# Kernel tuning notes

Measured on AMD Instinct MI355X. Metric: run time of the kernel, lower is better.

Reference implementation:

```python
import jax, jax.numpy as jnp
import numpy as np

K, D, E = 2048, 128, 64

def setup_inputs() -> dict:
    key = jax.random.key(0)
    k1, k2, k3 = jax.random.split(key, 3)
    z = jax.random.normal(k1, (K, D), dtype=jnp.float32)
    # Kaiming-like scaling so logits stay in a sane range
    W1 = jax.random.normal(k2, (2 * D, E), dtype=jnp.float32) / jnp.sqrt(2.0 * D)
    b1 = jnp.zeros((E,), dtype=jnp.float32)
    W2 = jax.random.normal(k3, (E, 1), dtype=jnp.float32) / jnp.sqrt(1.0 * E)
    b2 = jnp.zeros((1,), dtype=jnp.float32)
    return {"z": z, "W1": W1, "b1": b1, "W2": W2, "b2": b2}


def reference(z, W1, b1, W2, b2):
    # edge_mlp(cat([z_i, z_j])) == z_i @ W1[:d] + z_j @ W1[d:] + b1  (avoids (k,k,2d) concat)
    d = z.shape[1]
    hi = z @ W1[:d]          # (k, e)  -- contribution of z_i (row/query)
    hj = z @ W1[d:]          # (k, e)  -- contribution of z_j (col/key)
    h = jax.nn.silu(hi[:, None, :] + hj[None, :, :] + b1)   # (k, k, e)
    logits = jnp.einsum('ije,eo->ij', h, W2) + b2[0]         # (k, k)
    return jax.nn.softmax(logits, axis=-1)
```

## Files before the change

### kernel.cpp

```cpp
#include <hip/hip_runtime.h>
#include <cstdint>
#include <cstddef>

#define KTOT 2048
#define DDIM 128
#define EDIM 64
#define RPB  4
#define JR   512
#define KPB  4

#define LOG2E 1.44269504088896f

typedef float v2f __attribute__((ext_vector_type(2)));

__global__ void proj_kernel(const float* __restrict__ z,
                            const float* __restrict__ W1,
                            const float* __restrict__ b1,
                            const float* __restrict__ w2,
                            float* __restrict__ hiw, float* __restrict__ Ei,
                            float* __restrict__ hjw, float* __restrict__ Ej) {
  __shared__ float zrow[KPB][DDIM];
  const int t  = threadIdx.x;
  const int k0 = blockIdx.x * KPB;
#pragma unroll
  for (int r = 0; r < KPB; ++r) zrow[r][t] = z[(size_t)(k0 + r) * DDIM + t];
  __syncthreads();

  const int  e    = t & 63;
  const bool isHj = (t >= 64);
  const float* Wcol = W1 + (isHj ? DDIM * EDIM : 0) + e;

  float acc[KPB];
  const float binit = isHj ? 0.0f : b1[e];
#pragma unroll
  for (int r = 0; r < KPB; ++r) acc[r] = binit;

#pragma unroll 4
  for (int d = 0; d < DDIM; ++d) {
    const float w = Wcol[(size_t)d * EDIM];
#pragma unroll
    for (int r = 0; r < KPB; ++r) acc[r] = fmaf(zrow[r][d], w, acc[r]);
  }

  const float wv = w2[e];
  float* dw = isHj ? hjw : hiw;
  float* dE = isHj ? Ej  : Ei;
#pragma unroll
  for (int r = 0; r < KPB; ++r) {
    const float tv = acc[r] * LOG2E;
    dw[(size_t)(k0 + r) * EDIM + e] = tv * wv;
    dE[(size_t)(k0 + r) * EDIM + e] = __builtin_amdgcn_exp2f(-tv);
  }
}

__device__ __forceinline__ void quad_nd(const float4 hw, const float4 he,
                                        const float4 jw, const float4 je,
                                        float& Nq, float& Dq) {
  const v2f u01 = (v2f){hw.x, hw.y} + (v2f){jw.x, jw.y};
  const v2f u23 = (v2f){hw.z, hw.w} + (v2f){jw.z, jw.w};
  const v2f d01 = (v2f){he.x, he.y} * (v2f){je.x, je.y} + 1.0f;
  const v2f d23 = (v2f){he.z, he.w} * (v2f){je.z, je.w} + 1.0f;
  const float n01 = fmaf(u01.x, d01.y, u01.y * d01.x);
  const float n23 = fmaf(u23.x, d23.y, u23.y * d23.x);
  const float p01 = d01.x * d01.y;
  const float p23 = d23.x * d23.y;
  Nq = fmaf(n01, p23, n23 * p01);
  Dq = p01 * p23;
}

__device__ __forceinline__ float dpp_red8(float a) {
  int t;
  t = __builtin_amdgcn_update_dpp(0, __float_as_int(a), 0xB1, 0xF, 0xF, true);
  a += __int_as_float(t);
  t = __builtin_amdgcn_update_dpp(0, __float_as_int(a), 0x4E, 0xF, 0xF, true);
  a += __int_as_float(t);
  t = __builtin_amdgcn_update_dpp(0, __float_as_int(a), 0x141, 0xF, 0xF, true);
  a += __int_as_float(t);
  return a;
}

__global__ __launch_bounds__(256, 4) void edge_kernel(
    const float* __restrict__ hiw_, const float* __restrict__ Ei_,
    const float* __restrict__ hjw_, const float* __restrict__ Ej_,
    float* __restrict__ out, float* __restrict__ partials) {
  __shared__ float logits[RPB][JR];

  const int tid  = threadIdx.x;
  const int lane = tid & 63;
  const int wave = tid >> 6;
  const int sub  = lane & 7;
  const int jg   = lane >> 3;
  const int ig   = blockIdx.x >> 2;
  const int jq   = blockIdx.x & 3;
  const int i0   = ig * RPB;

  float4 hwA[RPB], hwB[RPB], heA[RPB], heB[RPB];
#pragma unroll
  for (int r = 0; r < RPB; ++r) {
    const size_t o = (size_t)(i0 + r) * EDIM + sub * 8;
    hwA[r] = *reinterpret_cast<const float4*>(hiw_ + o);
    hwB[r] = *reinterpret_cast<const float4*>(hiw_ + o + 4);
    heA[r] = *reinterpret_cast<const float4*>(Ei_ + o);
    heB[r] = *reinterpret_cast<const float4*>(Ei_ + o + 4);
  }

  const int jloc = wave * 8 + jg;
  const float* pjw = hjw_ + (size_t)(jq * JR + jloc) * EDIM + sub * 8;
  const float* pje = Ej_  + (size_t)(jq * JR + jloc) * EDIM + sub * 8;

  float4 jwA = *reinterpret_cast<const float4*>(pjw);
  float4 jwB = *reinterpret_cast<const float4*>(pjw + 4);
  float4 jeA = *reinterpret_cast<const float4*>(pje);
  float4 jeB = *reinterpret_cast<const float4*>(pje + 4);

  for (int it = 0; it < JR / 32; ++it) {
    const float4 cwA = jwA, cwB = jwB, ceA = jeA, ceB = jeB;
    if (it + 1 < JR / 32) {
      const size_t off = (size_t)(it + 1) * 32 * EDIM;
      jwA = *reinterpret_cast<const float4*>(pjw + off);
      jwB = *reinterpret_cast<const float4*>(pjw + off + 4);
      jeA = *reinterpret_cast<const float4*>(pje + off);
      jeB = *reinterpret_cast<const float4*>(pje + off + 4);
    }
    const int j = jloc + it * 32;
#pragma unroll
    for (int r = 0; r < RPB; ++r) {
      float N0, D0, N1, D1;
      quad_nd(hwA[r], heA[r], cwA, ceA, N0, D0);
      quad_nd(hwB[r], heB[r], cwB, ceB, N1, D1);
      const float rD = __builtin_amdgcn_rcpf(D0 * D1);
      float a = fmaf(N0, D1, N1 * D0) * rD;
      a = dpp_red8(a);
      if (sub == 0) logits[r][j] = a;
    }
  }
  __syncthreads();

  float* lrow = logits[wave];
  float ssum = 0.0f;
#pragma unroll
  for (int t = 0; t < 8; ++t) {
    const int k = t * 64 + lane;
    const float ev = __builtin_amdgcn_exp2f(lrow[k]);
    lrow[k] = ev;
    ssum += ev;
  }
#pragma unroll
  for (int off = 32; off; off >>= 1) ssum += __shfl_xor(ssum, off);
  if (lane == 0) partials[(size_t)(i0 + wave) * 4 + jq] = ssum;

  float* orow = out + (size_t)(i0 + wave) * KTOT + jq * JR;
#pragma unroll
  for (int t = 0; t < 2; ++t) {
    const int k4 = t * 64 + lane;
    *reinterpret_cast<float4*>(&orow[k4 * 4]) =
        *reinterpret_cast<const float4*>(&lrow[k4 * 4]);
  }
}

__global__ __launch_bounds__(256) void norm_kernel(
    const float* __restrict__ partials, float* __restrict__ out) {
  const int idx = blockIdx.x * 256 + threadIdx.x;
#pragma unroll
  for (int t = 0; t < 4; ++t) {
    const int i4  = idx + t * (1024 * 256);
    const int row = i4 >> 9;
    const float s = (partials[row * 4 + 0] + partials[row * 4 + 1]) +
                    (partials[row * 4 + 2] + partials[row * 4 + 3]);
    const float rinv = __builtin_amdgcn_rcpf(s);
    float4 v = reinterpret_cast<const float4*>(out)[i4];
    v.x *= rinv; v.y *= rinv; v.z *= rinv; v.w *= rinv;
    reinterpret_cast<float4*>(out)[i4] = v;
  }
}

extern "C" void kernel_launch(void* const* d_in, const int* in_sizes, int n_in,
                              void* d_out, int out_size, void* d_ws, size_t ws_size,
                              hipStream_t stream) {
  const float* z  = (const float*)d_in[0];
  const float* W1 = (const float*)d_in[1];
  const float* b1 = (const float*)d_in[2];
  const float* W2 = (const float*)d_in[3];
  float* out = (float*)d_out;

  float* hiw = (float*)d_ws;
  float* Ei  = hiw + (size_t)KTOT * EDIM;
  float* hjw = Ei  + (size_t)KTOT * EDIM;
  float* Ej  = hjw + (size_t)KTOT * EDIM;
  float* partials = Ej + (size_t)KTOT * EDIM;

  hipLaunchKernelGGL(proj_kernel, dim3(KTOT / KPB), dim3(DDIM), 0, stream,
                     z, W1, b1, W2, hiw, Ei, hjw, Ej);
  hipLaunchKernelGGL(edge_kernel, dim3((KTOT / RPB) * 4), dim3(256), 0, stream,
                     hiw, Ei, hjw, Ej, out, partials);
  hipLaunchKernelGGL(norm_kernel, dim3(1024), dim3(256), 0, stream,
                     partials, out);
}
```

Baseline: 62.32 us.

## Fuse softmax normalization into edge kernel with full-row blocks

Each block now covers 2 complete rows across all 2048 columns instead of 4 rows over a quarter of the columns. The block computes the exponentials inline, accumulates per-row sums in registers and shared memory, then rescales its own rows in place, so the separate norm kernel and partials buffer go away. This removes one launch and a full extra read/write pass over the 16 MB output. In exchange, the hj/Ej data is reloaded per 2 rows instead of per 4, which doubles L2 traffic. Output writes also become scattered scalar stores instead of coalesced float4 stores through LDS.

```diff
diff --git a/kernel.cpp b/kernel.cpp
--- a/kernel.cpp
+++ b/kernel.cpp
@@ -5,8 +5,7 @@
 #define KTOT 2048
 #define DDIM 128
 #define EDIM 64
-#define RPB  4
-#define JR   512
+#define RPB  2
 #define KPB  4
 
 #define LOG2E 1.44269504088896f
@@ -82,17 +81,15 @@
 __global__ __launch_bounds__(256, 4) void edge_kernel(
     const float* __restrict__ hiw_, const float* __restrict__ Ei_,
     const float* __restrict__ hjw_, const float* __restrict__ Ej_,
-    float* __restrict__ out, float* __restrict__ partials) {
-  __shared__ float logits[RPB][JR];
+    float* __restrict__ out) {
+  __shared__ float ps[4][RPB];
 
   const int tid  = threadIdx.x;
   const int lane = tid & 63;
   const int wave = tid >> 6;
   const int sub  = lane & 7;
   const int jg   = lane >> 3;
-  const int ig   = blockIdx.x >> 2;
-  const int jq   = blockIdx.x & 3;
-  const int i0   = ig * RPB;
+  const int i0   = blockIdx.x * RPB;
 
   float4 hwA[RPB], hwB[RPB], heA[RPB], heB[RPB];
 #pragma unroll
@@ -105,17 +102,20 @@
   }
 
   const int jloc = wave * 8 + jg;
-  const float* pjw = hjw_ + (size_t)(jq * JR + jloc) * EDIM + sub * 8;
-  const float* pje = Ej_  + (size_t)(jq * JR + jloc) * EDIM + sub * 8;
+  const float* pjw = hjw_ + (size_t)jloc * EDIM + sub * 8;
+  const float* pje = Ej_  + (size_t)jloc * EDIM + sub * 8;
 
   float4 jwA = *reinterpret_cast<const float4*>(pjw);
   float4 jwB = *reinterpret_cast<const float4*>(pjw + 4);
   float4 jeA = *reinterpret_cast<const float4*>(pje);
   float4 jeB = *reinterpret_cast<const float4*>(pje + 4);
 
-  for (int it = 0; it < JR / 32; ++it) {
+  float ssum[RPB] = {0.0f, 0.0f};
+  float* orow0 = out + (size_t)i0 * KTOT;
+
+  for (int it = 0; it < KTOT / 32; ++it) {
     const float4 cwA = jwA, cwB = jwB, ceA = jeA, ceB = jeB;
-    if (it + 1 < JR / 32) {
+    if (it + 1 < KTOT / 32) {
       const size_t off = (size_t)(it + 1) * 32 * EDIM;
       jwA = *reinterpret_cast<const float4*>(pjw + off);
       jwB = *reinterpret_cast<const float4*>(pjw + off + 4);
@@ -131,46 +131,32 @@
       const float rD = __builtin_amdgcn_rcpf(D0 * D1);
       float a = fmaf(N0, D1, N1 * D0) * rD;
       a = dpp_red8(a);
-      if (sub == 0) logits[r][j] = a;
+      const float ev = __builtin_amdgcn_exp2f(a);
+      ssum[r] += ev;
+      if (sub == 0) orow0[(size_t)r * KTOT + j] = ev;
     }
+  }
+
+#pragma unroll
+  for (int r = 0; r < RPB; ++r)
+#pragma unroll
+    for (int off = 32; off; off >>= 1) ssum[r] += __shfl_xor(ssum[r], off);
+  if (lane == 0) {
+#pragma unroll
+    for (int r = 0; r < RPB; ++r) ps[wave][r] = ssum[r];
   }
   __syncthreads();
 
-  float* lrow = logits[wave];
-  float ssum = 0.0f;
-#pragma unroll
-  for (int t = 0; t < 8; ++t) {
-    const int k = t * 64 + lane;
-    const float ev = __builtin_amdgcn_exp2f(lrow[k]);
-    lrow[k] = ev;
-    ssum += ev;
-  }
-#pragma unroll
-  for (int off = 32; off; off >>= 1) ssum += __shfl_xor(ssum, off);
-  if (lane == 0) partials[(size_t)(i0 + wave) * 4 + jq] = ssum;
-
-  float* orow = out + (size_t)(i0 + wave) * KTOT + jq * JR;
-#pragma unroll
-  for (int t = 0; t < 2; ++t) {
-    const int k4 = t * 64 + lane;
-    *reinterpret_cast<float4*>(&orow[k4 * 4]) =
-        *reinterpret_cast<const float4*>(&lrow[k4 * 4]);
-  }
-}
-
-__global__ __launch_bounds__(256) void norm_kernel(
-    const float* __restrict__ partials, float* __restrict__ out) {
-  const int idx = blockIdx.x * 256 + threadIdx.x;
+  const int r = wave >> 1;
+  const int h = wave & 1;
+  const float S = (ps[0][r] + ps[1][r]) + (ps[2][r] + ps[3][r]);
+  const float rinv = 8.0f * __builtin_amdgcn_rcpf(S);
+  float* orow = out + (size_t)(i0 + r) * KTOT + h * 1024;
 #pragma unroll
   for (int t = 0; t < 4; ++t) {
-    const int i4  = idx + t * (1024 * 256);
-    const int row = i4 >> 9;
-    const float s = (partials[row * 4 + 0] + partials[row * 4 + 1]) +
-                    (partials[row * 4 + 2] + partials[row * 4 + 3]);
-    const float rinv = __builtin_amdgcn_rcpf(s);
-    float4 v = reinterpret_cast<const float4*>(out)[i4];
+    float4 v = *reinterpret_cast<const float4*>(&orow[t * 256 + lane * 4]);
     v.x *= rinv; v.y *= rinv; v.z *= rinv; v.w *= rinv;
-    reinterpret_cast<float4*>(out)[i4] = v;
+    *reinterpret_cast<float4*>(&orow[t * 256 + lane * 4]) = v;
   }
 }
 
@@ -187,12 +173,9 @@
   float* Ei  = hiw + (size_t)KTOT * EDIM;
   float* hjw = Ei  + (size_t)KTOT * EDIM;
   float* Ej  = hjw + (size_t)KTOT * EDIM;
-  float* partials = Ej + (size_t)KTOT * EDIM;
 
   hipLaunchKernelGGL(proj_kernel, dim3(KTOT / KPB), dim3(DDIM), 0, stream,
                      z, W1, b1, W2, hiw, Ei, hjw, Ej);
-  hipLaunchKernelGGL(edge_kernel, dim3((KTOT / RPB) * 4), dim3(256), 0, stream,
-                     hiw, Ei, hjw, Ej, out, partials);
-  hipLaunchKernelGGL(norm_kernel, dim3(1024), dim3(256), 0, stream,
-                     partials, out);
+  hipLaunchKernelGGL(edge_kernel, dim3(KTOT / RPB), dim3(256), 0, stream,
+                     hiw, Ei, hjw, Ej, out);
 }
```

Measured after the change: 68.54 us. 10.0% more time.
